# Optimization experiments

Hardware: AMD Instinct MI355X
Metric: run time of the kernel (lower is better)

The kernel has to match this reference:

```python
import jax, jax.numpy as jnp
import numpy as np

INPUT_DIM = 2051
OUTPUT_DIM = 128
HEAD_SLICES = [(0, 1), (1, 2), (2, 3)]
HIDDEN = 100
HEAD_HIDDEN = 50
EPS = 1e-5
N = 65536

_head_cols = set()
for _s, _e in HEAD_SLICES:
    _head_cols.update(range(_s, _e))
NET_COLS = np.array([i for i in range(INPUT_DIM) if i not in _head_cols])
NET_DIM = len(NET_COLS)

_lens = [max(_e - _s, 2) for _s, _e in HEAD_SLICES]

def _build_combinations(lens):
    # lexicographic enumeration matching the recursive combs() in the torch code
    grids = np.stack(np.meshgrid(*[np.arange(l) for l in lens], indexing='ij'), -1).reshape(-1, len(lens))
    return np.concatenate([(grids[:, k:k + 1] == np.arange(l)[None]).astype(np.int32)
                           for k, l in enumerate(lens)], 1)

COMB = jnp.asarray(_build_combinations(_lens))  # [H, sum(lens)]
N_HEADS = int(COMB.shape[0])


def setup_inputs() -> dict:
    key = jax.random.key(0)
    ks = jax.random.split(key, 10)
    x = jax.random.normal(ks[0], (N, INPUT_DIM), jnp.float32)
    return {
        'x': x,
        'bn0_mean': jax.random.normal(ks[1], (NET_DIM,), jnp.float32) * 0.1,
        'bn0_var': jax.random.uniform(ks[2], (NET_DIM,), jnp.float32) + 0.5,
        'W_net': jax.random.normal(ks[3], (NET_DIM, HIDDEN), jnp.float32) / np.sqrt(NET_DIM).astype(np.float32),
        'b_net': jnp.zeros((HIDDEN,), jnp.float32),
        'bn1_mean': jax.random.normal(ks[4], (HIDDEN,), jnp.float32) * 0.1,
        'bn1_var': jax.random.uniform(ks[5], (HIDDEN,), jnp.float32) + 0.5,
        'W1': jax.random.normal(ks[6], (N_HEADS, HIDDEN, HEAD_HIDDEN), jnp.float32) / np.sqrt(HIDDEN).astype(np.float32),
        'b1': jnp.zeros((N_HEADS, HEAD_HIDDEN), jnp.float32),
        'bn2_mean': jax.random.normal(ks[7], (N_HEADS, HEAD_HIDDEN), jnp.float32) * 0.1,
        'bn2_var': jax.random.uniform(ks[8], (N_HEADS, HEAD_HIDDEN), jnp.float32) + 0.5,
        'W2': jax.random.normal(ks[9], (N_HEADS, HEAD_HIDDEN, OUTPUT_DIM), jnp.float32) / np.sqrt(HEAD_HIDDEN).astype(np.float32),
        'b2': jnp.zeros((N_HEADS, OUTPUT_DIM), jnp.float32),
    }


def reference(x, bn0_mean, bn0_var, W_net, b_net, bn1_mean, bn1_var,
              W1, b1, bn2_mean, bn2_var, W2, b2):
    # --- routing: build one-hot combination bits per row and match to COMB ---
    parts = []
    for s, e in HEAD_SLICES:
        t = x[:, s:e]
        if e - s == 1:
            t = jnp.concatenate([1.0 - t, t], axis=1)
        parts.append(t)
    comb = (jnp.concatenate(parts, axis=1) > 0.5).astype(jnp.int32)        # [n, sum(lens)]
    comb_idx = jnp.argmax(jnp.all(comb[:, None, :] == COMB[None], axis=-1), axis=1)  # [n]

    # --- trunk net: BN (no affine, eval) -> Linear -> (Dropout=id) -> ReLU -> BN ---
    xn = jnp.take(x, jnp.asarray(NET_COLS), axis=1)                        # [n, NET_DIM]
    h = (xn - bn0_mean) * jax.lax.rsqrt(bn0_var + EPS)
    h = jax.nn.relu(h @ W_net + b_net)
    h = (h - bn1_mean) * jax.lax.rsqrt(bn1_var + EPS)                      # [n, 100]

    # --- per-head MLPs, computed as batched small GEMMs then per-row select ---
    h1 = jax.nn.relu(jnp.einsum('nd,hdo->hno', h, W1) + b1[:, None, :])    # [H, n, 50]
    h1 = (h1 - bn2_mean[:, None, :]) * jax.lax.rsqrt(bn2_var[:, None, :] + EPS)
    out_all = jnp.einsum('hno,hod->hnd', h1, W2) + b2[:, None, :]          # [H, n, D]
    out = jnp.take_along_axis(out_all.transpose(1, 0, 2),
                              comb_idx[:, None, None], axis=1)[:, 0]        # [n, D]
    return out
```

## Files before the change

kernel.cpp:

```cpp
#include <hip/hip_runtime.h>

typedef __attribute__((ext_vector_type(8))) short short8;
typedef __attribute__((ext_vector_type(4))) float float4v;
typedef unsigned short ushort_t;

#define N_SAMPLES 65536
#define IN_DIM 2051
#define NET_K 2048
#define NPAD 128
#define EPSV 1e-5f

static constexpr size_t OFF_WT  = 0;
static constexpr size_t OFF_BP  = 524288;
static constexpr size_t OFF_B1F = 524800;
static constexpr size_t OFF_W1F = 526400;
static constexpr size_t OFF_W2F = 686400;
static constexpr size_t OFF_B2F = 891200;
static constexpr size_t OFF_CNT = 895296;
static constexpr size_t OFF_BKT = 895360;
static constexpr size_t OFF_H   = 2992512;

__device__ __forceinline__ ushort_t f2bf(float f) {
    union { float f; unsigned u; } c; c.f = f;
    unsigned r = (c.u + 0x7FFFu + ((c.u >> 16) & 1u)) >> 16;
    return (ushort_t)r;
}

__global__ void fold_wnet(const float* __restrict__ W_net, const float* __restrict__ var0,
                          ushort_t* __restrict__ WT) {
    int id = blockIdx.x * 256 + threadIdx.x;
    int k = id & 2047, n = id >> 11;
    float v = 0.f;
    if (n < 100) v = W_net[k * 100 + n] * rsqrtf(var0[k] + EPSV);
    WT[(size_t)n * 2048 + k] = f2bf(v);
}

__global__ void fold_bnet(const float* __restrict__ W_net, const float* __restrict__ mean0,
                          const float* __restrict__ var0, const float* __restrict__ b_net,
                          float* __restrict__ bp) {
    int j = blockIdx.x, t = threadIdx.x;
    __shared__ float red[256];
    float s = 0.f;
    if (j < 100)
        for (int k = t; k < NET_K; k += 256)
            s += mean0[k] * rsqrtf(var0[k] + EPSV) * W_net[k * 100 + j];
    red[t] = s; __syncthreads();
    for (int w = 128; w > 0; w >>= 1) { if (t < w) red[t] += red[t + w]; __syncthreads(); }
    if (t == 0) bp[j] = (j < 100) ? (b_net[j] - red[0]) : 0.f;
}

__global__ void fold_heads(const float* __restrict__ m1, const float* __restrict__ v1,
                           const float* __restrict__ W1, const float* __restrict__ b1,
                           const float* __restrict__ m2, const float* __restrict__ v2,
                           const float* __restrict__ W2, const float* __restrict__ b2,
                           float* __restrict__ W1f, float* __restrict__ b1f,
                           float* __restrict__ W2f, float* __restrict__ b2f) {
    int hd = blockIdx.x, t = threadIdx.x;
    const float* W1h = W1 + hd * 5000; float* W1fh = W1f + hd * 5000;
    for (int id = t; id < 5000; id += 256) {
        int k = id / 50;
        W1fh[id] = rsqrtf(v1[k] + EPSV) * W1h[id];
    }
    if (t < 50) {
        float s = 0.f;
        for (int k = 0; k < 100; k++) s += m1[k] * rsqrtf(v1[k] + EPSV) * W1h[k * 50 + t];
        b1f[hd * 50 + t] = b1[hd * 50 + t] - s;
    }
    const float* W2h = W2 + hd * 6400; float* W2fh = W2f + hd * 6400;
    const float* m2h = m2 + hd * 50;   const float* v2h = v2 + hd * 50;
    for (int id = t; id < 6400; id += 256) {
        int o = id >> 7;
        W2fh[id] = rsqrtf(v2h[o] + EPSV) * W2h[id];
    }
    if (t < 128) {
        float s = 0.f;
        for (int o = 0; o < 50; o++) s += m2h[o] * rsqrtf(v2h[o] + EPSV) * W2h[o * 128 + t];
        b2f[hd * 128 + t] = b2[hd * 128 + t] - s;
    }
}

__global__ __launch_bounds__(256) void bin_heads(const float* __restrict__ x,
                                                 int* __restrict__ cnt,
                                                 int* __restrict__ bkt) {
    __shared__ int lcnt[8];
    __shared__ int lbase[8];
    int t = threadIdx.x;
    if (t < 8) lcnt[t] = 0;
    __syncthreads();
    int sid = blockIdx.x * 256 + t;
    const float* xr = x + (size_t)sid * IN_DIM;
    float x0 = xr[0], x1 = xr[1], x2 = xr[2];
    bool b0 = x0 > 0.5f, b1 = x1 > 0.5f, b2 = x2 > 0.5f;
    bool l0 = (1.0f - x0) > 0.5f, l1 = (1.0f - x1) > 0.5f, l2 = (1.0f - x2) > 0.5f;
    int idx;
    if ((l0 || b0) && (l1 || b1) && (l2 || b2))
        idx = (b0 ? 4 : 0) | (b1 ? 2 : 0) | (b2 ? 1 : 0);
    else
        idx = 0;
    int pos = atomicAdd(&lcnt[idx], 1);
    __syncthreads();
    if (t < 8) lbase[t] = atomicAdd(&cnt[t], lcnt[t]);
    __syncthreads();
    bkt[idx * N_SAMPLES + lbase[idx] + pos] = sid;
}

__global__ __launch_bounds__(256, 4) void gemm1(const float* __restrict__ x,
                                                const ushort_t* __restrict__ WT,
                                                const float* __restrict__ bp,
                                                float* __restrict__ h) {
    const int tid = threadIdx.x;
    const int wave = tid >> 6, lane = tid & 63;
    const int lrow = lane & 15;
    const int lquad = lane >> 4;
    const int mBase = blockIdx.x * 64 + wave * 16;
    const float* xrow = x + (size_t)(mBase + lrow) * IN_DIM + 3;

    float4v acc[8];
    const float4v zero4 = {0.f, 0.f, 0.f, 0.f};
#pragma unroll
    for (int i = 0; i < 8; i++) acc[i] = zero4;

    for (int ks = 0; ks < 64; ++ks) {
        const int k0 = ks * 32 + lquad * 8;
        const float* ap = xrow + k0;
        short8 afrag;
#pragma unroll
        for (int j = 0; j < 8; ++j) afrag[j] = (short)f2bf(ap[j]);
#pragma unroll
        for (int nt = 0; nt < 8; ++nt) {
            short8 bfrag = *(const short8*)(WT + (size_t)(nt * 16 + lrow) * 2048 + k0);
            acc[nt] = __builtin_amdgcn_mfma_f32_16x16x32_bf16(afrag, bfrag, acc[nt], 0, 0, 0);
        }
    }
#pragma unroll
    for (int nt = 0; nt < 8; ++nt) {
        int n = nt * 16 + lrow;
        float bv = bp[n];
#pragma unroll
        for (int r = 0; r < 4; ++r) {
            int m = mBase + lquad * 4 + r;
            float v = acc[nt][r] + bv;
            h[(size_t)m * NPAD + n] = v > 0.f ? v : 0.f;
        }
    }
}

__global__ __launch_bounds__(256) void heads_mlp(const float* __restrict__ h,
                                                 const int* __restrict__ cnt,
                                                 const int* __restrict__ bkt,
                                                 const float* __restrict__ W1f,
                                                 const float* __restrict__ b1f,
                                                 const float* __restrict__ W2f,
                                                 const float* __restrict__ b2f,
                                                 float* __restrict__ out) {
    int hd = blockIdx.x >> 8;
    int slot = (blockIdx.x & 255) * 256 + threadIdx.x;
    if (slot >= cnt[hd]) return;
    int sid = bkt[hd * N_SAMPLES + slot];
    const float* hv = h + (size_t)sid * NPAD;
    const float* W1h = W1f + hd * 5000;
    const float* b1h = b1f + hd * 50;

    float t1[50];
#pragma unroll
    for (int j = 0; j < 50; j++) t1[j] = b1h[j];
    const float4v* hv4 = (const float4v*)hv;
    for (int k4 = 0; k4 < 25; k4++) {
        float4v hk = hv4[k4];
#pragma unroll
        for (int jj = 0; jj < 4; jj++) {
            float hkj = hk[jj];
#pragma unroll
            for (int j = 0; j < 50; j++) t1[j] += hkj * W1h[(k4 * 4 + jj) * 50 + j];
        }
    }
#pragma unroll
    for (int j = 0; j < 50; j++) t1[j] = t1[j] > 0.f ? t1[j] : 0.f;

    const float* W2h = W2f + hd * 6400;
    const float* b2h = b2f + hd * 128;
    float* op = out + (size_t)sid * 128;
#pragma unroll 1
    for (int c = 0; c < 4; c++) {
        float acc[32];
#pragma unroll
        for (int o = 0; o < 32; o++) acc[o] = b2h[c * 32 + o];
        for (int j = 0; j < 50; j++) {
            float tj = t1[j];
#pragma unroll
            for (int o = 0; o < 32; o++) acc[o] += tj * W2h[j * 128 + c * 32 + o];
        }
        float4v* op4 = (float4v*)(op + c * 32);
#pragma unroll
        for (int q = 0; q < 8; q++) {
            float4v v = {acc[4 * q], acc[4 * q + 1], acc[4 * q + 2], acc[4 * q + 3]};
            op4[q] = v;
        }
    }
}

extern "C" void kernel_launch(void* const* d_in, const int* in_sizes, int n_in,
                              void* d_out, int out_size, void* d_ws, size_t ws_size,
                              hipStream_t stream) {
    const float* x        = (const float*)d_in[0];
    const float* bn0_mean = (const float*)d_in[1];
    const float* bn0_var  = (const float*)d_in[2];
    const float* W_net    = (const float*)d_in[3];
    const float* b_net    = (const float*)d_in[4];
    const float* bn1_mean = (const float*)d_in[5];
    const float* bn1_var  = (const float*)d_in[6];
    const float* W1       = (const float*)d_in[7];
    const float* b1       = (const float*)d_in[8];
    const float* bn2_mean = (const float*)d_in[9];
    const float* bn2_var  = (const float*)d_in[10];
    const float* W2       = (const float*)d_in[11];
    const float* b2       = (const float*)d_in[12];
    float* out = (float*)d_out;
    char* ws = (char*)d_ws;

    ushort_t* WT  = (ushort_t*)(ws + OFF_WT);
    float* BP     = (float*)(ws + OFF_BP);
    float* B1F    = (float*)(ws + OFF_B1F);
    float* W1F    = (float*)(ws + OFF_W1F);
    float* W2F    = (float*)(ws + OFF_W2F);
    float* B2F    = (float*)(ws + OFF_B2F);
    int*   CNT    = (int*)(ws + OFF_CNT);
    int*   BKT    = (int*)(ws + OFF_BKT);
    float* H      = (float*)(ws + OFF_H);

    hipMemsetAsync(ws + OFF_CNT, 0, 64, stream);
    fold_wnet<<<1024, 256, 0, stream>>>(W_net, bn0_var, WT);
    fold_bnet<<<128, 256, 0, stream>>>(W_net, bn0_mean, bn0_var, b_net, BP);
    fold_heads<<<8, 256, 0, stream>>>(bn1_mean, bn1_var, W1, b1,
                                      bn2_mean, bn2_var, W2, b2,
                                      W1F, B1F, W2F, B2F);
    bin_heads<<<N_SAMPLES / 256, 256, 0, stream>>>(x, CNT, BKT);
    gemm1<<<N_SAMPLES / 64, 256, 0, stream>>>(x, WT, BP, H);
    heads_mlp<<<8 * 256, 256, 0, stream>>>(H, CNT, BKT, W1F, B1F, W2F, B2F, out);
}
```

Baseline: 1.074 ms.

## Double-buffer gemm1 operand loads in registers and drop unused eighth N tile

Restructures the gemm1 main loop into a two-stage register pipeline. The x and weight fragments for the next k-step are loaded while MFMAs run on the current step, to hide global load latency. It also cuts the N tiles from 8 to 7, since 112 columns still cover the 100 hidden units, saving MFMAs and weight loads. The cost is higher register pressure from two sets of buffers, which may lower occupancy under the 4-blocks launch bound. Columns 112-127 of h are no longer written, which is only safe if later stages ignore them.

```diff
diff --git a/kernel.cpp b/kernel.cpp
--- a/kernel.cpp
+++ b/kernel.cpp
@@ -113,27 +113,62 @@
     const int lrow = lane & 15;
     const int lquad = lane >> 4;
     const int mBase = blockIdx.x * 64 + wave * 16;
-    const float* xrow = x + (size_t)(mBase + lrow) * IN_DIM + 3;
-
-    float4v acc[8];
-    const float4v zero4 = {0.f, 0.f, 0.f, 0.f};
-#pragma unroll
-    for (int i = 0; i < 8; i++) acc[i] = zero4;
-
-    for (int ks = 0; ks < 64; ++ks) {
-        const int k0 = ks * 32 + lquad * 8;
-        const float* ap = xrow + k0;
-        short8 afrag;
-#pragma unroll
-        for (int j = 0; j < 8; ++j) afrag[j] = (short)f2bf(ap[j]);
-#pragma unroll
-        for (int nt = 0; nt < 8; ++nt) {
-            short8 bfrag = *(const short8*)(WT + (size_t)(nt * 16 + lrow) * 2048 + k0);
-            acc[nt] = __builtin_amdgcn_mfma_f32_16x16x32_bf16(afrag, bfrag, acc[nt], 0, 0, 0);
-        }
-    }
-#pragma unroll
-    for (int nt = 0; nt < 8; ++nt) {
+    const float* xrow = x + (size_t)(mBase + lrow) * IN_DIM + 3 + lquad * 8;
+    const ushort_t* wrow = WT + (size_t)lrow * 2048 + lquad * 8;
+
+    float4v acc[7];
+#pragma unroll
+    for (int i = 0; i < 7; i++) acc[i] = (float4v){0.f, 0.f, 0.f, 0.f};
+
+    float a0[8], a1[8];
+    short8 bb0[7], bb1[7];
+
+#pragma unroll
+    for (int j = 0; j < 8; ++j) a0[j] = xrow[j];
+#pragma unroll
+    for (int nt = 0; nt < 7; ++nt)
+        bb0[nt] = *(const short8*)(wrow + (size_t)nt * (16 * 2048));
+
+    for (int ks = 0; ks < 64; ks += 2) {
+        {
+            const float* ap = xrow + (ks + 1) * 32;
+            const ushort_t* bpp = wrow + (ks + 1) * 32;
+#pragma unroll
+            for (int j = 0; j < 8; ++j) a1[j] = ap[j];
+#pragma unroll
+            for (int nt = 0; nt < 7; ++nt)
+                bb1[nt] = *(const short8*)(bpp + (size_t)nt * (16 * 2048));
+        }
+        {
+            short8 af;
+#pragma unroll
+            for (int j = 0; j < 8; ++j) af[j] = (short)f2bf(a0[j]);
+#pragma unroll
+            for (int nt = 0; nt < 7; ++nt)
+                acc[nt] = __builtin_amdgcn_mfma_f32_16x16x32_bf16(af, bb0[nt], acc[nt], 0, 0, 0);
+        }
+        {
+            const int kp = (ks + 2 < 64) ? ks + 2 : 63;
+            const float* ap = xrow + kp * 32;
+            const ushort_t* bpp = wrow + kp * 32;
+#pragma unroll
+            for (int j = 0; j < 8; ++j) a0[j] = ap[j];
+#pragma unroll
+            for (int nt = 0; nt < 7; ++nt)
+                bb0[nt] = *(const short8*)(bpp + (size_t)nt * (16 * 2048));
+        }
+        {
+            short8 af;
+#pragma unroll
+            for (int j = 0; j < 8; ++j) af[j] = (short)f2bf(a1[j]);
+#pragma unroll
+            for (int nt = 0; nt < 7; ++nt)
+                acc[nt] = __builtin_amdgcn_mfma_f32_16x16x32_bf16(af, bb1[nt], acc[nt], 0, 0, 0);
+        }
+    }
+
+#pragma unroll
+    for (int nt = 0; nt < 7; ++nt) {
         int n = nt * 16 + lrow;
         float bv = bp[n];
 #pragma unroll
```

Result: faster. 1.036 ms (-3.5%).
